# Performance work log

Hardware: AMD Instinct MI355X
Metric: run time of the kernel (lower is better)

Reference implementation:

```python
import jax, jax.numpy as jnp
import numpy as np

DIM = 1024
HEADS = 16
DIM_HEAD = DIM // HEADS
SCALE = DIM_HEAD ** -0.5
LN_EPS = 1e-5


def setup_inputs() -> dict:
    key = jax.random.key(0)
    ks = jax.random.split(key, 7)
    b, n = 4, 2048
    x = jax.random.normal(ks[0], (b, n, DIM), dtype=jnp.float32)
    pos = jax.random.normal(ks[1], (b, n, DIM), dtype=jnp.float32)
    # params (torch Linear init-like scale)
    w_qkv = jax.random.normal(ks[2], (DIM, 3 * DIM), dtype=jnp.float32) * (DIM ** -0.5)
    w_out = jax.random.normal(ks[3], (DIM, DIM), dtype=jnp.float32) * (DIM ** -0.5)
    b_out = jax.random.normal(ks[4], (DIM,), dtype=jnp.float32) * 0.01
    ln_gamma = jnp.ones((DIM,), dtype=jnp.float32)
    ln_beta = jnp.zeros((DIM,), dtype=jnp.float32)
    return {"x": x, "pos": pos, "w_qkv": w_qkv, "w_out": w_out,
            "b_out": b_out, "ln_gamma": ln_gamma, "ln_beta": ln_beta}


def _layer_norm(x, gamma, beta):
    mu = jnp.mean(x, axis=-1, keepdims=True)
    var = jnp.mean(jnp.square(x - mu), axis=-1, keepdims=True)
    return (x - mu) * jax.lax.rsqrt(var + LN_EPS) * gamma + beta


def reference(x, pos, w_qkv, w_out, b_out, ln_gamma, ln_beta):
    b, n, _ = x.shape
    xn = _layer_norm(x, ln_gamma, ln_beta)
    qkv = xn @ w_qkv                                    # [b, n, 3*dim]
    q, k, v = jnp.split(qkv, 3, axis=-1)
    # [b, n, dim] -> [b, h, n, d]
    to_heads = lambda t: t.reshape(b, n, HEADS, DIM_HEAD).transpose(0, 2, 1, 3)
    q, k, v = to_heads(q), to_heads(k), to_heads(v)
    scores = jnp.einsum('bhid,bhjd->bhij', q, k) * SCALE  # [b, h, n, n]
    attn = jax.nn.softmax(scores, axis=-1)
    out = jnp.einsum('bhij,bhjd->bhid', attn, v)          # [b, h, n, d]
    out = out.transpose(0, 2, 1, 3).reshape(b, n, DIM)    # [b, n, dim]
    return (out + pos) @ w_out + b_out
```

## Files before the change

kernel.cpp:

```cpp
#include <hip/hip_runtime.h>
#include <math.h>
#include <stdint.h>

#define TOKENS 8192
#define DIM 1024
#define N3 3072
#define NSEQ 2048
#define NH 16
#define DH 64

typedef __attribute__((ext_vector_type(8))) __bf16 bf16x8;
typedef __attribute__((ext_vector_type(4))) float f32x4;
typedef __attribute__((ext_vector_type(16))) float f32x16;
typedef __attribute__((ext_vector_type(4))) short short4v;

__device__ __forceinline__ unsigned cvt2bf(float a, float b) {
    unsigned r;
    asm("v_cvt_pk_bf16_f32 %0, %1, %2" : "=v"(r) : "v"(a), "v"(b));
    return r;
}
__device__ __forceinline__ unsigned short f2bf(float f) {
    unsigned r;
    asm("v_cvt_pk_bf16_f32 %0, %1, %1" : "=v"(r) : "v"(f));
    return (unsigned short)r;
}
__device__ __forceinline__ float exp2_raw(float x) {
    float r;
    asm("v_exp_f32 %0, %1" : "=v"(r) : "v"(x));
    return r;
}

__device__ __forceinline__ void glds16(const void* g, void* l) {
    __builtin_amdgcn_global_load_lds((__attribute__((address_space(1))) void*)(void*)g,
                                     (__attribute__((address_space(3))) void*)l, 16, 0, 0);
}

__global__ __launch_bounds__(256) void transpose_to_bf16(
    const float* __restrict__ in, unsigned short* __restrict__ out, int R, int C) {
    __shared__ float tile[64][65];
    int n0 = blockIdx.x * 64, k0 = blockIdx.y * 64;
    int t = threadIdx.x;
#pragma unroll
    for (int i = 0; i < 16; i++) {
        int idx = i * 256 + t;
        int r = idx >> 6, c = idx & 63;
        tile[r][c] = in[(size_t)(k0 + r) * C + n0 + c];
    }
    __syncthreads();
#pragma unroll
    for (int i = 0; i < 16; i++) {
        int idx = i * 256 + t;
        int r = idx >> 6, c = idx & 63;
        out[(size_t)(n0 + r) * R + k0 + c] = f2bf(tile[c][r]);
    }
}

__global__ __launch_bounds__(256) void ln_kernel(
    const float* __restrict__ x, const float* __restrict__ gamma,
    const float* __restrict__ beta, unsigned short* __restrict__ xn) {
    int row = blockIdx.x;
    int t = threadIdx.x;
    const float4 v = ((const float4*)(x + (size_t)row * DIM))[t];
    float s = v.x + v.y + v.z + v.w;
    float sq = v.x * v.x + v.y * v.y + v.z * v.z + v.w * v.w;
#pragma unroll
    for (int m = 1; m < 64; m <<= 1) {
        s += __shfl_xor(s, m);
        sq += __shfl_xor(sq, m);
    }
    __shared__ float ws[4], wq[4];
    int w = t >> 6, lane = t & 63;
    if (lane == 0) { ws[w] = s; wq[w] = sq; }
    __syncthreads();
    s = ws[0] + ws[1] + ws[2] + ws[3];
    sq = wq[0] + wq[1] + wq[2] + wq[3];
    float mu = s * (1.0f / DIM);
    float var = sq * (1.0f / DIM) - mu * mu;
    float rstd = rsqrtf(var + 1e-5f);
    const float4 g = ((const float4*)gamma)[t];
    const float4 bb = ((const float4*)beta)[t];
    uint2 o;
    o.x = cvt2bf((v.x - mu) * rstd * g.x + bb.x, (v.y - mu) * rstd * g.y + bb.y);
    o.y = cvt2bf((v.z - mu) * rstd * g.z + bb.z, (v.w - mu) * rstd * g.w + bb.w);
    *(uint2*)(xn + (size_t)row * DIM + t * 4) = o;
}

__device__ __forceinline__ void xcd_swizzle(int& bx, int& by) {
    int nwgx = gridDim.x;
    int nwg = nwgx * gridDim.y;
    int wg = by * nwgx + bx;
    int cpx = nwg >> 3;
    int swz = (wg & 7) * cpx + (wg >> 3);
    bx = swz % nwgx;
    by = swz / nwgx;
}

__device__ __forceinline__ void gemm_core8(
    const unsigned short* __restrict__ A, const unsigned short* __restrict__ Bt, int K,
    int brow, int bcol, char* As, char* Bs, f32x4 acc[2][4]) {
    int t = threadIdx.x, w = t >> 6, lane = t & 63;
    int wm = w >> 1, wn = w & 1;
    int srow = lane >> 2, scol = (lane & 3) * 8;
    const char* sA = (const char*)(A + (size_t)(brow + w * 16 + srow) * K + scol);
    const char* sB = (const char*)(Bt + (size_t)(bcol + w * 16 + srow) * K + scol);
    char* a0 = As; char* a1 = As + 8192; char* a2 = As + 16384;
    char* b0 = Bs; char* b1 = Bs + 8192; char* b2 = Bs + 16384;
    auto stage = [&](int k0, char* ab, char* bb) {
        glds16(sA + (size_t)k0 * 2, ab + w * 1024);
        glds16(sB + (size_t)k0 * 2, bb + w * 1024);
    };
    stage(0, a0, b0);
    stage(32, a1, b1);
    int NT = K >> 5;
    for (int kt = 0; kt < NT; kt++) {
        asm volatile("s_waitcnt vmcnt(2)" ::: "memory");
        __builtin_amdgcn_s_barrier();
        int kn = kt + 2; if (kn >= NT) kn -= NT;
        stage(kn << 5, a2, b2);
        bf16x8 a[2], b[4];
#pragma unroll
        for (int i = 0; i < 2; i++)
            a[i] = *(const bf16x8*)(a0 + (wm * 32 + i * 16 + (lane & 15)) * 64 + (lane >> 4) * 16);
#pragma unroll
        for (int j = 0; j < 4; j++)
            b[j] = *(const bf16x8*)(b0 + (wn * 64 + j * 16 + (lane & 15)) * 64 + (lane >> 4) * 16);
        __builtin_amdgcn_s_setprio(1);
#pragma unroll
        for (int i = 0; i < 2; i++)
#pragma unroll
            for (int j = 0; j < 4; j++)
                acc[i][j] = __builtin_amdgcn_mfma_f32_16x16x32_bf16(a[i], b[j], acc[i][j], 0, 0, 0);
        __builtin_amdgcn_s_setprio(0);
        char* tp;
        tp = a0; a0 = a1; a1 = a2; a2 = tp;
        tp = b0; b0 = b1; b1 = b2; b2 = tp;
    }
}

#define QSCALE_LOG2E 0.18033688011112042f

__global__ __launch_bounds__(512, 6) void gemm_qkv(
    const unsigned short* __restrict__ A, const unsigned short* __restrict__ Bt,
    unsigned short* __restrict__ Qb, unsigned short* __restrict__ Kb,
    unsigned short* __restrict__ Vt) {
    __shared__ __align__(16) char As[3 * 8192];
    __shared__ __align__(16) char Bs[3 * 8192];
    int bx = blockIdx.x, by = blockIdx.y;
    xcd_swizzle(bx, by);
    int brow = by * 128, bcol = bx * 128;
    f32x4 acc[2][4] = {};
    gemm_core8(A, Bt, DIM, brow, bcol, As, Bs, acc);

    int t = threadIdx.x, w = t >> 6, lane = t & 63;
    int wm = w >> 1, wn = w & 1;
    int part = bcol >> 10;
#pragma unroll
    for (int i = 0; i < 2; i++) {
#pragma unroll
        for (int j = 0; j < 4; j++) {
            int col = bcol + wn * 64 + j * 16 + (lane & 15);
            int within = col & 1023;
            int h = within >> 6, d = within & 63;
            int rowb = brow + wm * 32 + i * 16 + (lane >> 4) * 4;
            if (part == 2) {
                int b = rowb >> 11, n = rowb & 2047;
                int bh = (b << 4) + h;
                uint2 pv;
                pv.x = cvt2bf(acc[i][j][0], acc[i][j][1]);
                pv.y = cvt2bf(acc[i][j][2], acc[i][j][3]);
                *(uint2*)(Vt + ((size_t)bh * 64 + d) * 2048 + n) = pv;
            } else {
#pragma unroll
                for (int r = 0; r < 4; r++) {
                    int row = rowb + r;
                    int b = row >> 11, n = row & 2047;
                    int bh = (b << 4) + h;
                    float val = acc[i][j][r];
                    if (part == 0)
                        Qb[((size_t)bh * 2048 + n) * 64 + d] = f2bf(val * QSCALE_LOG2E);
                    else
                        Kb[((size_t)bh * 2048 + n) * 64 + d] = f2bf(val);
                }
            }
        }
    }
}

__global__ __launch_bounds__(512, 6) void gemm_out(
    const unsigned short* __restrict__ A, const unsigned short* __restrict__ Bt,
    const float* __restrict__ bias, float* __restrict__ out) {
    __shared__ __align__(16) char As[3 * 8192];
    __shared__ __align__(16) char Bs[3 * 8192];
    int bx = blockIdx.x, by = blockIdx.y;
    xcd_swizzle(bx, by);
    int brow = by * 128, bcol = bx * 128;
    f32x4 acc[2][4] = {};
    gemm_core8(A, Bt, DIM, brow, bcol, As, Bs, acc);

    int t = threadIdx.x, w = t >> 6, lane = t & 63;
    int wm = w >> 1, wn = w & 1;
#pragma unroll
    for (int i = 0; i < 2; i++) {
#pragma unroll
        for (int j = 0; j < 4; j++) {
            int col = bcol + wn * 64 + j * 16 + (lane & 15);
            float bv = bias[col];
#pragma unroll
            for (int r = 0; r < 4; r++) {
                int row = brow + wm * 32 + i * 16 + (lane >> 4) * 4 + r;
                out[(size_t)row * DIM + col] = acc[i][j][r] + bv;
            }
        }
    }
}

__global__ __launch_bounds__(512, 4) void attn_kernel(
    const unsigned short* __restrict__ Qb, const unsigned short* __restrict__ Kb,
    const unsigned short* __restrict__ Vt, const float* __restrict__ pos,
    unsigned short* __restrict__ att) {
    __shared__ __align__(16) char KV[4][8192];
    int t = threadIdx.x, w = t >> 6, lane = t & 63;
    int l31 = lane & 31, lhi = lane >> 5;

    int L = blockIdx.y * gridDim.x + blockIdx.x;
    int bh = (L & 7) + (((L >> 3) & 7) << 3);
    int qt = L >> 6;
    int b = bh >> 4, h = bh & 15;
    int qr = qt * 256 + w * 32 + l31;

    const unsigned short* Qh = Qb + (size_t)bh * NSEQ * DH;
    const char* Khc = (const char*)(Kb + (size_t)bh * NSEQ * DH);
    const char* Vhc = (const char*)(Vt + (size_t)bh * DH * NSEQ);

    bf16x8 qf[4];
#pragma unroll
    for (int ks = 0; ks < 4; ks++)
        qf[ks] = *(const bf16x8*)(Qh + (size_t)qr * DH + ks * 16 + lhi * 8);

    f32x16 oacc[2] = {};
    f32x16 oextra = {};
    unsigned one2 = 0x3F803F80u;
    uint4 onew = {one2, one2, one2, one2};
    bf16x8 onesf = *(bf16x8*)&onew;

    const char* srcBase;
    size_t strideT;
    if (w < 4) {
        srcBase = Khc + (size_t)l31 * 128 + w * 32 + lhi * 16;
        strideT = 32 * 128;
    } else {
        int c = w - 4, dt = c >> 1, ks = c & 1;
        srcBase = Vhc + (size_t)(dt * 32 + l31) * 4096 + (size_t)(ks * 16 + lhi * 8) * 2;
        strideT = 32 * 2;
    }
    auto stage = [&](char* buf, int tl) {
        glds16(srcBase + (size_t)tl * strideT, buf + w * 1024);
    };

    auto QK = [&](const char* kc) -> f32x16 {
        f32x16 s = {};
#pragma unroll
        for (int ks = 0; ks < 4; ks++) {
            bf16x8 kf = *(const bf16x8*)(kc + ks * 1024 + lane * 16);
            s = __builtin_amdgcn_mfma_f32_32x32x16_bf16(kf, qf[ks], s, 0, 0, 0);
        }
        return s;
    };

    auto FIN = [&](f32x16& sv, const char* vc) {
#pragma unroll
        for (int r = 0; r < 16; r++) sv[r] = exp2_raw(sv[r]);
        bf16x8 bfr[2];
#pragma unroll
        for (int ks = 0; ks < 2; ks++) {
            int rb = ks * 8;
            unsigned pa = cvt2bf(sv[rb + 0], sv[rb + 1]);
            unsigned pc = cvt2bf(sv[rb + 2], sv[rb + 3]);
            unsigned pb = cvt2bf(sv[rb + 4], sv[rb + 5]);
            unsigned pd = cvt2bf(sv[rb + 6], sv[rb + 7]);
            asm("v_permlane32_swap_b32 %0, %1" : "+v"(pa), "+v"(pb));
            asm("v_permlane32_swap_b32 %0, %1" : "+v"(pc), "+v"(pd));
            uint4 pw = {pa, pc, pb, pd};
            bfr[ks] = *(bf16x8*)&pw;
        }
        __builtin_amdgcn_s_setprio(1);
#pragma unroll
        for (int ks = 0; ks < 2; ks++) {
#pragma unroll
            for (int dt = 0; dt < 2; dt++) {
                bf16x8 vf = *(const bf16x8*)(vc + 4096 + (dt * 2 + ks) * 1024 + lane * 16);
                oacc[dt] = __builtin_amdgcn_mfma_f32_32x32x16_bf16(vf, bfr[ks], oacc[dt], 0, 0, 0);
            }
            oextra = __builtin_amdgcn_mfma_f32_32x32x16_bf16(onesf, bfr[ks], oextra, 0, 0, 0);
        }
        __builtin_amdgcn_s_setprio(0);
    };

    char* q0 = KV[0]; char* q1 = KV[1]; char* q2 = KV[2]; char* q3 = KV[3];
    stage(q0, 0); stage(q1, 1); stage(q2, 2);
    asm volatile("s_waitcnt vmcnt(2)" ::: "memory");
    __builtin_amdgcn_s_barrier();
    f32x16 sP = QK(q0);
    f32x16 sN;

    for (int tl = 0; tl < 64; tl += 2) {
        asm volatile("s_waitcnt vmcnt(1)" ::: "memory");
        __builtin_amdgcn_s_barrier();
        stage(q3, (tl + 3) & 63);
        sN = QK(q1);
        FIN(sP, q0);
        asm volatile("s_waitcnt vmcnt(1)" ::: "memory");
        __builtin_amdgcn_s_barrier();
        stage(q0, (tl + 4) & 63);
        sP = QK(q2);
        FIN(sN, q1);
        char* tp0 = q0; char* tp1 = q1;
        q0 = q2; q1 = q3; q2 = tp0; q3 = tp1;
    }

    float lsum = oextra[0];
    float inv = 1.0f / lsum;
    size_t rowbase = ((size_t)b * NSEQ + qr) * DIM + h * 64;
#pragma unroll
    for (int dt = 0; dt < 2; dt++)
#pragma unroll
        for (int g4 = 0; g4 < 4; g4++) {
            int d = dt * 32 + g4 * 8 + lhi * 4;
            float4 pv = *(const float4*)(pos + rowbase + d);
            uint2 o;
            o.x = cvt2bf(oacc[dt][g4 * 4 + 0] * inv + pv.x, oacc[dt][g4 * 4 + 1] * inv + pv.y);
            o.y = cvt2bf(oacc[dt][g4 * 4 + 2] * inv + pv.z, oacc[dt][g4 * 4 + 3] * inv + pv.w);
            *(uint2*)(att + rowbase + d) = o;
        }
}

extern "C" void kernel_launch(void* const* d_in, const int* in_sizes, int n_in,
                              void* d_out, int out_size, void* d_ws, size_t ws_size,
                              hipStream_t stream) {
    const float* x = (const float*)d_in[0];
    const float* pos = (const float*)d_in[1];
    const float* w_qkv = (const float*)d_in[2];
    const float* w_out = (const float*)d_in[3];
    const float* b_out = (const float*)d_in[4];
    const float* ln_g = (const float*)d_in[5];
    const float* ln_b = (const float*)d_in[6];
    float* out = (float*)d_out;

    char* ws = (char*)d_ws;
    unsigned short* xn      = (unsigned short*)(ws);
    unsigned short* wqkv_bt = (unsigned short*)(ws + (16ull << 20));
    unsigned short* wout_bt = (unsigned short*)(ws + (22ull << 20));
    unsigned short* Qb      = (unsigned short*)(ws + (24ull << 20));
    unsigned short* Kb      = (unsigned short*)(ws + (40ull << 20));
    unsigned short* Vt      = (unsigned short*)(ws + (56ull << 20));
    unsigned short* att     = xn;

    transpose_to_bf16<<<dim3(N3 / 64, DIM / 64), 256, 0, stream>>>(w_qkv, wqkv_bt, DIM, N3);
    transpose_to_bf16<<<dim3(DIM / 64, DIM / 64), 256, 0, stream>>>(w_out, wout_bt, DIM, DIM);
    ln_kernel<<<TOKENS, 256, 0, stream>>>(x, ln_g, ln_b, xn);
    gemm_qkv<<<dim3(N3 / 128, TOKENS / 128), 512, 0, stream>>>(xn, wqkv_bt, Qb, Kb, Vt);
    attn_kernel<<<dim3(NSEQ / 256, 64), 512, 0, stream>>>(Qb, Kb, Vt, pos, att);
    gemm_out<<<dim3(DIM / 128, TOKENS / 128), 512, 0, stream>>>(att, wout_bt, b_out, out);
}
```

Measured before the change: 196.6 us.

## Restructure attention KV pipeline to six-buffer, two-tile-per-barrier staging

Replaces the four-buffer software pipeline, where QK of the next tile overlapped with the softmax/PV of the previous tile, with a six-buffer ring that stages two tiles per iteration. Each iteration now needs one barrier instead of two. The cost is that QK and FIN run back-to-back without interleaving, which removes the MFMA/softmax overlap. LDS use per block grows from 32KB to 48KB, which could limit occupancy at 512 threads with launch_bounds 4.

After: 195.9 us. No clear change (-0.3%).

```diff
diff --git a/kernel.cpp b/kernel.cpp
--- a/kernel.cpp
+++ b/kernel.cpp
@@ -218,7 +218,7 @@
     const unsigned short* __restrict__ Qb, const unsigned short* __restrict__ Kb,
     const unsigned short* __restrict__ Vt, const float* __restrict__ pos,
     unsigned short* __restrict__ att) {
-    __shared__ __align__(16) char KV[4][8192];
+    __shared__ __align__(16) char KV[6][8192];
     int t = threadIdx.x, w = t >> 6, lane = t & 63;
     int l31 = lane & 31, lhi = lane >> 5;
 
@@ -296,26 +296,25 @@
         __builtin_amdgcn_s_setprio(0);
     };
 
-    char* q0 = KV[0]; char* q1 = KV[1]; char* q2 = KV[2]; char* q3 = KV[3];
-    stage(q0, 0); stage(q1, 1); stage(q2, 2);
-    asm volatile("s_waitcnt vmcnt(2)" ::: "memory");
-    __builtin_amdgcn_s_barrier();
-    f32x16 sP = QK(q0);
-    f32x16 sN;
-
-    for (int tl = 0; tl < 64; tl += 2) {
-        asm volatile("s_waitcnt vmcnt(1)" ::: "memory");
+    char* pA0 = KV[0]; char* pA1 = KV[1];
+    char* pB0 = KV[2]; char* pB1 = KV[3];
+    char* pC0 = KV[4]; char* pC1 = KV[5];
+    stage(pA0, 0); stage(pA1, 1);
+    stage(pB0, 2); stage(pB1, 3);
+
+    for (int i = 0; i < 32; i++) {
+        asm volatile("s_waitcnt vmcnt(2)" ::: "memory");
         __builtin_amdgcn_s_barrier();
-        stage(q3, (tl + 3) & 63);
-        sN = QK(q1);
-        FIN(sP, q0);
-        asm volatile("s_waitcnt vmcnt(1)" ::: "memory");
-        __builtin_amdgcn_s_barrier();
-        stage(q0, (tl + 4) & 63);
-        sP = QK(q2);
-        FIN(sN, q1);
-        char* tp0 = q0; char* tp1 = q1;
-        q0 = q2; q1 = q3; q2 = tp0; q3 = tp1;
+        int tn = (2 * i + 4) & 63;
+        stage(pC0, tn); stage(pC1, tn + 1);
+        f32x16 s0 = QK(pA0);
+        FIN(s0, pA0);
+        f32x16 s1 = QK(pA1);
+        FIN(s1, pA1);
+        char* t0 = pA0; char* t1 = pA1;
+        pA0 = pB0; pA1 = pB1;
+        pB0 = pC0; pB1 = pC1;
+        pC0 = t0;  pC1 = t1;
     }
 
     float lsum = oextra[0];
```
